# Optimization experiments

Hardware: AMD Instinct MI355X
Metric: run time of the kernel (lower is better)

Reference implementation:

```python
import jax, jax.numpy as jnp
import numpy as np

B, IN, H0, H1, OUT = 4096, 1024, 4096, 4096, 1024
QMAX = 127.0


def setup_inputs() -> dict:
    key = jax.random.key(0)
    k0, k1, k2, k3 = jax.random.split(key, 4)
    x = jax.random.normal(k0, (B, IN), dtype=jnp.float32)
    # Linear weights hold already-quantized integer values (module casts .int())
    W0 = jax.random.randint(k1, (H0, IN + 1), -127, 128).astype(jnp.int32)
    W1 = jax.random.randint(k2, (H1, H0 + 1), -127, 128).astype(jnp.int32)
    W2 = jax.random.randint(k3, (OUT, H1 + 1), -127, 128).astype(jnp.int32)
    return {
        "x": x,
        "a_in0": jnp.float32(4.0), "a_w0": jnp.float32(0.05),
        "a_in2": jnp.float32(50.0), "a_w2": jnp.float32(0.05),
        "a_in4": jnp.float32(50.0), "a_w4": jnp.float32(0.05),
        "W0": W0, "W1": W1, "W2": W2,
    }


def _quant(x, amax):
    # clamp(round(x * 127/amax), -127, 127) -> int32
    return jnp.clip(jnp.round(x * (QMAX / amax)), -QMAX, QMAX).astype(jnp.int32)


def _qlinear(x, W, a_in, a_w):
    q = _quant(x, a_in)                                   # [B, K] int32
    ones = jnp.ones((q.shape[0], 1), dtype=jnp.int32)     # folded bias column
    q = jnp.concatenate([q, ones], axis=1)                # [B, K+1]
    acc = q @ W.T                                         # int32 GEMM [B, N]
    return acc.astype(jnp.float32) * (a_w * a_in / (QMAX * QMAX))


def reference(x, a_in0, a_w0, a_in2, a_w2, a_in4, a_w4, W0, W1, W2):
    x = x.reshape(x.shape[0], -1)
    x = _qlinear(x, W0, a_in0, a_w0)
    x = jax.nn.relu(x)
    x = _qlinear(x, W1, a_in2, a_w2)
    x = jax.nn.relu(x)
    x = _qlinear(x, W2, a_in4, a_w4)
    return x
```

## Files before the change

### kernel.cpp

```cpp
#include <hip/hip_runtime.h>

#define QMAX 127.0f

typedef int v4i __attribute__((ext_vector_type(4)));

__device__ __forceinline__ void gload_lds16(const void* g, void* l) {
  __builtin_amdgcn_global_load_lds(
      (const __attribute__((address_space(1))) void*)g,
      (__attribute__((address_space(3))) void*)l, 16, 0, 0);
}

__device__ __forceinline__ void pack_body(const int* __restrict__ W,
                                          signed char* __restrict__ W8,
                                          int* __restrict__ bias,
                                          unsigned lblk, int kshift) {
  unsigned t = lblk * 256u + threadIdx.x;
  unsigned row = t >> kshift;
  unsigned j = t & ((1u << kshift) - 1u);
  unsigned K = 4u << kshift;
  size_t srcBase = (size_t)row * (size_t)(K + 1) + (size_t)j * 4;
  int c0 = W[srcBase + 0], c1 = W[srcBase + 1], c2 = W[srcBase + 2], c3 = W[srcBase + 3];
  unsigned packed = (unsigned)(c0 & 0xff) | ((unsigned)(c1 & 0xff) << 8) |
                    ((unsigned)(c2 & 0xff) << 16) | ((unsigned)(c3 & 0xff) << 24);
  reinterpret_cast<unsigned*>(W8)[t] = packed;
  if (j == 0) bias[row] = W[(size_t)row * (K + 1) + K];
}

__global__ void prep_kernel(const float* __restrict__ x,
                            signed char* __restrict__ qa0,
                            const float* __restrict__ pAin,
                            const int* __restrict__ W0, signed char* __restrict__ W0p, int* __restrict__ b0,
                            const int* __restrict__ W1, signed char* __restrict__ W1p, int* __restrict__ b1,
                            const int* __restrict__ W2, signed char* __restrict__ W2p, int* __restrict__ b2) {
  unsigned blk = blockIdx.x;
  if (blk < 4096u) {
    pack_body(W0, W0p, b0, blk, 8);
  } else if (blk < 20480u) {
    pack_body(W1, W1p, b1, blk - 4096u, 10);
  } else if (blk < 24576u) {
    pack_body(W2, W2p, b2, blk - 20480u, 10);
  } else {
    unsigned t = (blk - 24576u) * 256u + threadIdx.x;
    float s = QMAX / pAin[0];
    float4 v = reinterpret_cast<const float4*>(x)[t];
    int q0 = (int)fminf(fmaxf(rintf(v.x * s), -QMAX), QMAX);
    int q1 = (int)fminf(fmaxf(rintf(v.y * s), -QMAX), QMAX);
    int q2 = (int)fminf(fmaxf(rintf(v.z * s), -QMAX), QMAX);
    int q3 = (int)fminf(fmaxf(rintf(v.w * s), -QMAX), QMAX);
    unsigned packed = (unsigned)(q0 & 0xff) | ((unsigned)(q1 & 0xff) << 8) |
                      ((unsigned)(q2 & 0xff) << 16) | ((unsigned)(q3 & 0xff) << 24);
    reinterpret_cast<unsigned*>(qa0)[t] = packed;
  }
}


#define FENCE() asm volatile("" ::: "memory")
#define BARRIER()                      \
  do {                                 \
    FENCE();                           \
    __builtin_amdgcn_s_barrier();      \
    FENCE();                           \
  } while (0)
#define LGK(n) asm volatile("s_waitcnt lgkmcnt(" #n ")" ::: "memory")
#define VMC(n) asm volatile("s_waitcnt vmcnt(" #n ")" ::: "memory")

#define STG128(bf, t)                                                         \
  do {                                                                        \
    _Pragma("unroll") for (int ii = 0; ii < 4; ++ii) {                        \
      int c = ii * 256 + tid;                                                 \
      int r = c >> 3;                                                         \
      int osrc = ((c & 7) << 4) ^ ((r & 7) << 4);                             \
      gload_lds16(A + (size_t)(browBase + r) * K + ((t) * 128 + osrc),        \
                  ldsA + (bf) * 16384 + c * 16);                              \
      gload_lds16(Bw + (size_t)(bcolBase + r) * K + ((t) * 128 + osrc),       \
                  ldsB + (bf) * 16384 + c * 16);                              \
    }                                                                         \
  } while (0)

#define LDA4_128(bf, kk, dst)                                                 \
  do {                                                                        \
    _Pragma("unroll") for (int m = 0; m < 4; ++m) {                           \
      int row = wr + m * 16 + l15;                                            \
      int off = ((kk) * 64 + hi * 16) ^ ((l15 & 7) << 4);                     \
      dst[m] = *(const v4i*)(ldsA + (bf) * 16384 + row * 128 + off);          \
    }                                                                         \
  } while (0)

#define LDB4_128(bf, kk)                                                      \
  do {                                                                        \
    _Pragma("unroll") for (int n = 0; n < 4; ++n) {                           \
      int row = wc + n * 16 + l15;                                            \
      int off = ((kk) * 64 + hi * 16) ^ ((l15 & 7) << 4);                     \
      bK[n] = *(const v4i*)(ldsB + (bf) * 16384 + row * 128 + off);           \
    }                                                                         \
  } while (0)

#define MFMA16(aset)                                                          \
  do {                                                                        \
    __builtin_amdgcn_s_setprio(1);                                            \
    _Pragma("unroll") for (int m = 0; m < 4; ++m)                             \
    _Pragma("unroll") for (int n = 0; n < 4; ++n)                             \
      acc[m][n] = __builtin_amdgcn_mfma_i32_16x16x64_i8(                      \
          aset[m], bK[n], acc[m][n], 0, 0, 0);                                \
    __builtin_amdgcn_s_setprio(0);                                            \
  } while (0)

template <int MODE>
__global__ __launch_bounds__(256)
void qgemm_kernel(const signed char* __restrict__ A,
                  const signed char* __restrict__ Bw,
                  const int* __restrict__ bias,
                  void* __restrict__ outp,
                  int N, int K, int nbn,
                  const float* __restrict__ pAin,
                  const float* __restrict__ pAw,
                  const float* __restrict__ pAnext) {
  __shared__ signed char slds[65536];
  signed char* ldsA = slds;
  signed char* ldsB = slds + 32768;

  const int nwg = gridDim.x, bid = blockIdx.x, per = nwg >> 3;
  const int swz = (bid & 7) * per + (bid >> 3);
  const int brow = swz / nbn, bcol = swz - brow * nbn;
  const int browBase = brow << 7, bcolBase = bcol << 7;

  const int tid = threadIdx.x;
  const int lane = tid & 63, l15 = lane & 15, hi = lane >> 4;
  const int wid = tid >> 6;
  const int wr = (wid >> 1) << 6, wc = (wid & 1) << 6;

  v4i acc[4][4] = {};
  v4i aK0[4], aK1[4], bK[4];

  const int nk = K >> 7, niter = nk >> 1, nkm = nk - 1;

  STG128(0, 0);
  VMC(0);
  BARRIER();
  LDA4_128(0, 0, aK0);

#pragma unroll 1
  for (int i = 0; i < niter; ++i) {
    const int tO = 2 * i + 1;
    const int tE = (2 * i + 2) & nkm;
    LGK(4);
    BARRIER();
    STG128(1, tO);
    LDB4_128(0, 0); FENCE(); LDA4_128(0, 1, aK1);
    LGK(4);
    MFMA16(aK0);
    VMC(0);
    BARRIER();
    LDB4_128(0, 1); FENCE(); LDA4_128(1, 0, aK0);
    LGK(4);
    MFMA16(aK1);
    LGK(4);
    BARRIER();
    STG128(0, tE);
    LDB4_128(1, 0); FENCE(); LDA4_128(1, 1, aK1);
    LGK(4);
    MFMA16(aK0);
    VMC(0);
    BARRIER();
    LDB4_128(1, 1); FENCE(); LDA4_128(0, 0, aK0);
    LGK(4);
    MFMA16(aK1);
  }

  VMC(0);

  const float sDeq = (pAw[0] * pAin[0]) / (QMAX * QMAX);
  if (MODE == 0) {
    const float sQ = QMAX / pAnext[0];
    signed char* O = reinterpret_cast<signed char*>(outp);
#pragma unroll
    for (int n = 0; n < 4; ++n) {
      int gcol = bcolBase + wc + n * 16 + l15;
      int bv = bias[gcol];
#pragma unroll
      for (int m = 0; m < 4; ++m) {
        int growb = browBase + wr + m * 16 + (hi << 2);
#pragma unroll
        for (int r = 0; r < 4; ++r) {
          float f = (float)(acc[m][n][r] + bv) * sDeq;
          f = fmaxf(f, 0.0f);
          float qf = fminf(fmaxf(rintf(f * sQ), -QMAX), QMAX);
          O[(size_t)(growb + r) * N + gcol] = (signed char)(int)qf;
        }
      }
    }
  } else {
    float* O = reinterpret_cast<float*>(outp);
#pragma unroll
    for (int n = 0; n < 4; ++n) {
      int gcol = bcolBase + wc + n * 16 + l15;
      int bv = bias[gcol];
#pragma unroll
      for (int m = 0; m < 4; ++m) {
        int growb = browBase + wr + m * 16 + (hi << 2);
#pragma unroll
        for (int r = 0; r < 4; ++r) {
          O[(size_t)(growb + r) * N + gcol] = (float)(acc[m][n][r] + bv) * sDeq;
        }
      }
    }
  }
}

extern "C" void kernel_launch(void* const* d_in, const int* in_sizes, int n_in,
                              void* d_out, int out_size, void* d_ws, size_t ws_size,
                              hipStream_t stream) {
  const float* x     = (const float*)d_in[0];
  const float* a_in0 = (const float*)d_in[1];
  const float* a_w0  = (const float*)d_in[2];
  const float* a_in2 = (const float*)d_in[3];
  const float* a_w2  = (const float*)d_in[4];
  const float* a_in4 = (const float*)d_in[5];
  const float* a_w4  = (const float*)d_in[6];
  const int*   W0    = (const int*)d_in[7];
  const int*   W1    = (const int*)d_in[8];
  const int*   W2    = (const int*)d_in[9];
  float* out = (float*)d_out;

  constexpr int B = 4096, IN = 1024, H0 = 4096, H1 = 4096, OUTN = 1024;

  char* ws = (char*)d_ws;
  size_t off = 0;
  auto alloc = [&](size_t sz) {
    char* p = ws + off;
    off += (sz + 255) & ~(size_t)255;
    return p;
  };
  signed char* qa0 = (signed char*)alloc((size_t)B * IN);
  signed char* qa1 = (signed char*)alloc((size_t)B * H0);
  signed char* qa2 = (signed char*)alloc((size_t)B * H1);
  signed char* W0p = (signed char*)alloc((size_t)H0 * IN);
  signed char* W1p = (signed char*)alloc((size_t)H1 * H0);
  signed char* W2p = (signed char*)alloc((size_t)OUTN * H1);
  int* b0 = (int*)alloc((size_t)H0 * 4);
  int* b1 = (int*)alloc((size_t)H1 * 4);
  int* b2 = (int*)alloc((size_t)OUTN * 4);

  prep_kernel<<<28672, 256, 0, stream>>>(x, qa0, a_in0,
                                         W0, W0p, b0,
                                         W1, W1p, b1,
                                         W2, W2p, b2);

  qgemm_kernel<0><<<(B / 128) * (H0 / 128), 256, 0, stream>>>(
      qa0, W0p, b0, qa1, H0, IN, H0 / 128, a_in0, a_w0, a_in2);

  qgemm_kernel<0><<<(B / 128) * (H1 / 128), 256, 0, stream>>>(
      qa1, W1p, b1, qa2, H1, H0, H1 / 128, a_in2, a_w2, a_in4);

  qgemm_kernel<1><<<(B / 128) * (OUTN / 128), 256, 0, stream>>>(
      qa2, W2p, b2, out, OUTN, H1, OUTN / 128, a_in4, a_w4, a_in4);
}
```

Before: 148.1 us.

## Use 256x256 tiles with 128KB LDS for the two int8 ReLU-quant GEMMs

Adds a new int8 GEMM kernel with 256x256 output tiles per workgroup. Each wave owns a 128x128 sub-tile of 8x8 MFMA fragments, and the kernel uses 128KB of dynamic LDS with double-buffered A/B stages and register double-buffering of the fragments. The first two layers switch to this kernel to raise arithmetic intensity and cut global/LDS traffic per MFMA. The last fp32-output layer keeps the 128x128 kernel. The trade-offs are one workgroup per CU, far fewer workgroups (256 for 4096x4096), and heavy register pressure from 64 accumulators.

Result: no change. 148.5 us (+0.3%).

```diff
diff --git a/kernel.cpp b/kernel.cpp
--- a/kernel.cpp
+++ b/kernel.cpp
@@ -53,7 +53,6 @@
   }
 }
 
-
 #define FENCE() asm volatile("" ::: "memory")
 #define BARRIER()                      \
   do {                                 \
@@ -64,15 +63,137 @@
 #define LGK(n) asm volatile("s_waitcnt lgkmcnt(" #n ")" ::: "memory")
 #define VMC(n) asm volatile("s_waitcnt vmcnt(" #n ")" ::: "memory")
 
+
+#define STG4(gbase, ldsbuf, t)                                                \
+  do {                                                                        \
+    _Pragma("unroll") for (int s = 0; s < 8; ++s)                             \
+      gload_lds16(gbase + (size_t)(s * 32) * K + (size_t)(t) * 128,           \
+                  (ldsbuf) + s * 4096 + tid * 16);                            \
+  } while (0)
+
+#define LDA8k(bf, kk, dst)                                                    \
+  do {                                                                        \
+    _Pragma("unroll") for (int m = 0; m < 8; ++m) {                           \
+      int row = wm * 128 + m * 16 + l15;                                      \
+      int off = ((kk) * 64 + hi * 16) ^ ((row & 7) << 4);                     \
+      dst[m] = *(const v4i*)(ldsA + (bf) * 32768 + row * 128 + off);          \
+    }                                                                         \
+  } while (0)
+
+#define LDB8k(bf, kk, dst)                                                    \
+  do {                                                                        \
+    _Pragma("unroll") for (int n = 0; n < 8; ++n) {                           \
+      int row = wn * 128 + n * 16 + l15;                                      \
+      int off = ((kk) * 64 + hi * 16) ^ ((row & 7) << 4);                     \
+      dst[n] = *(const v4i*)(ldsB + (bf) * 32768 + row * 128 + off);          \
+    }                                                                         \
+  } while (0)
+
+#define MFMA64(aset, bset)                                                    \
+  do {                                                                        \
+    __builtin_amdgcn_s_setprio(1);                                            \
+    _Pragma("unroll") for (int m = 0; m < 8; ++m)                             \
+    _Pragma("unroll") for (int n = 0; n < 8; ++n)                             \
+      acc[m][n] = __builtin_amdgcn_mfma_i32_16x16x64_i8(                      \
+          aset[m], bset[n], acc[m][n], 0, 0, 0);                              \
+    __builtin_amdgcn_s_setprio(0);                                            \
+  } while (0)
+
+__global__ __launch_bounds__(256, 1)
+void qgemm4w_kernel(const signed char* __restrict__ A,
+                    const signed char* __restrict__ Bw,
+                    const int* __restrict__ bias,
+                    signed char* __restrict__ O,
+                    int N, int K, int nbn,
+                    const float* __restrict__ pAin,
+                    const float* __restrict__ pAw,
+                    const float* __restrict__ pAnext) {
+  extern __shared__ signed char lds[];
+  signed char* ldsA = lds;
+  signed char* ldsB = lds + 65536;
+
+  const int nwg = gridDim.x, bid = blockIdx.x, per = nwg >> 3;
+  const int swz = (bid & 7) * per + (bid >> 3);
+  const int brow = swz / nbn, bcol = swz - brow * nbn;
+  const int browBase = brow << 8, bcolBase = bcol << 8;
+
+  const int tid = threadIdx.x;
+  const int lane = tid & 63, l15 = lane & 15, hi = lane >> 4;
+  const int wid = tid >> 6, wm = wid >> 1, wn = wid & 1;
+
+  const int r0 = tid >> 3;
+  const int osrc = ((tid & 7) ^ (r0 & 7)) << 4;
+  const signed char* gA = A + (size_t)(browBase + r0) * K + osrc;
+  const signed char* gB = Bw + (size_t)(bcolBase + r0) * K + osrc;
+
+  v4i acc[8][8] = {};
+  v4i aR0[8], bR0[8], aR1[8], bR1[8];
+
+  const int nk = K >> 7, niter = nk >> 1, nkm = nk - 1;
+
+  STG4(gA, ldsA, 0); STG4(gB, ldsB, 0);
+  VMC(0);
+  BARRIER();
+  LDA8k(0, 0, aR0); LDB8k(0, 0, bR0);
+  STG4(gA, ldsA + 32768, 1); STG4(gB, ldsB + 32768, 1);
+
+#pragma unroll 1
+  for (int i = 0; i < niter; ++i) {
+    const int tE = (2 * i + 2) & nkm;
+    const int tN = (2 * i + 3) & nkm;
+    LDA8k(0, 1, aR1); LDB8k(0, 1, bR1);
+    LGK(15);
+    MFMA64(aR0, bR0);
+    VMC(0);
+    BARRIER();
+    LDA8k(1, 0, aR0); LDB8k(1, 0, bR0);
+    LGK(15);
+    MFMA64(aR1, bR1);
+    BARRIER();
+    STG4(gA, ldsA, tE); STG4(gB, ldsB, tE);
+    LDA8k(1, 1, aR1); LDB8k(1, 1, bR1);
+    LGK(15);
+    MFMA64(aR0, bR0);
+    VMC(0);
+    BARRIER();
+    LDA8k(0, 0, aR0); LDB8k(0, 0, bR0);
+    LGK(15);
+    MFMA64(aR1, bR1);
+    BARRIER();
+    STG4(gA, ldsA + 32768, tN); STG4(gB, ldsB + 32768, tN);
+  }
+
+  VMC(0); LGK(0);
+
+  const float sDeq = (pAw[0] * pAin[0]) / (QMAX * QMAX);
+  const float sQ = QMAX / pAnext[0];
+#pragma unroll
+  for (int nf = 0; nf < 8; ++nf) {
+    const int gcol = bcolBase + wn * 128 + nf * 16 + l15;
+    const int bv = bias[gcol];
+#pragma unroll
+    for (int mf = 0; mf < 8; ++mf) {
+      const int gr = browBase + wm * 128 + mf * 16 + (hi << 2);
+#pragma unroll
+      for (int r = 0; r < 4; ++r) {
+        float f = (float)(acc[mf][nf][r] + bv) * sDeq;
+        f = fmaxf(f, 0.0f);
+        float qf = fminf(fmaxf(rintf(f * sQ), -QMAX), QMAX);
+        O[(size_t)(gr + r) * N + gcol] = (signed char)(int)qf;
+      }
+    }
+  }
+}
+
 #define STG128(bf, t)                                                         \
   do {                                                                        \
     _Pragma("unroll") for (int ii = 0; ii < 4; ++ii) {                        \
       int c = ii * 256 + tid;                                                 \
       int r = c >> 3;                                                         \
-      int osrc = ((c & 7) << 4) ^ ((r & 7) << 4);                             \
-      gload_lds16(A + (size_t)(browBase + r) * K + ((t) * 128 + osrc),        \
+      int osrc2 = ((c & 7) << 4) ^ ((r & 7) << 4);                            \
+      gload_lds16(A + (size_t)(browBase + r) * K + ((t) * 128 + osrc2),       \
                   ldsA + (bf) * 16384 + c * 16);                              \
-      gload_lds16(Bw + (size_t)(bcolBase + r) * K + ((t) * 128 + osrc),       \
+      gload_lds16(Bw + (size_t)(bcolBase + r) * K + ((t) * 128 + osrc2),      \
                   ldsB + (bf) * 16384 + c * 16);                              \
     }                                                                         \
   } while (0)
@@ -81,7 +202,7 @@
   do {                                                                        \
     _Pragma("unroll") for (int m = 0; m < 4; ++m) {                           \
       int row = wr + m * 16 + l15;                                            \
-      int off = ((kk) * 64 + hi * 16) ^ ((l15 & 7) << 4);                     \
+      int off = ((kk) * 64 + hi * 16) ^ ((row & 7) << 4);                     \
       dst[m] = *(const v4i*)(ldsA + (bf) * 16384 + row * 128 + off);          \
     }                                                                         \
   } while (0)
@@ -90,7 +211,7 @@
   do {                                                                        \
     _Pragma("unroll") for (int n = 0; n < 4; ++n) {                           \
       int row = wc + n * 16 + l15;                                            \
-      int off = ((kk) * 64 + hi * 16) ^ ((l15 & 7) << 4);                     \
+      int off = ((kk) * 64 + hi * 16) ^ ((row & 7) << 4);                     \
       bK[n] = *(const v4i*)(ldsB + (bf) * 16384 + row * 128 + off);           \
     }                                                                         \
   } while (0)
@@ -105,16 +226,14 @@
     __builtin_amdgcn_s_setprio(0);                                            \
   } while (0)
 
-template <int MODE>
 __global__ __launch_bounds__(256)
 void qgemm_kernel(const signed char* __restrict__ A,
                   const signed char* __restrict__ Bw,
                   const int* __restrict__ bias,
-                  void* __restrict__ outp,
+                  float* __restrict__ O,
                   int N, int K, int nbn,
                   const float* __restrict__ pAin,
-                  const float* __restrict__ pAw,
-                  const float* __restrict__ pAnext) {
+                  const float* __restrict__ pAw) {
   __shared__ signed char slds[65536];
   signed char* ldsA = slds;
   signed char* ldsB = slds + 32768;
@@ -170,38 +289,16 @@
   VMC(0);
 
   const float sDeq = (pAw[0] * pAin[0]) / (QMAX * QMAX);
-  if (MODE == 0) {
-    const float sQ = QMAX / pAnext[0];
-    signed char* O = reinterpret_cast<signed char*>(outp);
-#pragma unroll
-    for (int n = 0; n < 4; ++n) {
-      int gcol = bcolBase + wc + n * 16 + l15;
-      int bv = bias[gcol];
-#pragma unroll
-      for (int m = 0; m < 4; ++m) {
-        int growb = browBase + wr + m * 16 + (hi << 2);
-#pragma unroll
-        for (int r = 0; r < 4; ++r) {
-          float f = (float)(acc[m][n][r] + bv) * sDeq;
-          f = fmaxf(f, 0.0f);
-          float qf = fminf(fmaxf(rintf(f * sQ), -QMAX), QMAX);
-          O[(size_t)(growb + r) * N + gcol] = (signed char)(int)qf;
-        }
-      }
-    }
-  } else {
-    float* O = reinterpret_cast<float*>(outp);
-#pragma unroll
-    for (int n = 0; n < 4; ++n) {
-      int gcol = bcolBase + wc + n * 16 + l15;
-      int bv = bias[gcol];
-#pragma unroll
-      for (int m = 0; m < 4; ++m) {
-        int growb = browBase + wr + m * 16 + (hi << 2);
-#pragma unroll
-        for (int r = 0; r < 4; ++r) {
-          O[(size_t)(growb + r) * N + gcol] = (float)(acc[m][n][r] + bv) * sDeq;
-        }
+#pragma unroll
+  for (int n = 0; n < 4; ++n) {
+    int gcol = bcolBase + wc + n * 16 + l15;
+    int bv = bias[gcol];
+#pragma unroll
+    for (int m = 0; m < 4; ++m) {
+      int growb = browBase + wr + m * 16 + (hi << 2);
+#pragma unroll
+      for (int r = 0; r < 4; ++r) {
+        O[(size_t)(growb + r) * N + gcol] = (float)(acc[m][n][r] + bv) * sDeq;
       }
     }
   }
@@ -241,17 +338,20 @@
   int* b1 = (int*)alloc((size_t)H1 * 4);
   int* b2 = (int*)alloc((size_t)OUTN * 4);
 
+  hipFuncSetAttribute((const void*)qgemm4w_kernel,
+                      hipFuncAttributeMaxDynamicSharedMemorySize, 131072);
+
   prep_kernel<<<28672, 256, 0, stream>>>(x, qa0, a_in0,
                                          W0, W0p, b0,
                                          W1, W1p, b1,
                                          W2, W2p, b2);
 
-  qgemm_kernel<0><<<(B / 128) * (H0 / 128), 256, 0, stream>>>(
-      qa0, W0p, b0, qa1, H0, IN, H0 / 128, a_in0, a_w0, a_in2);
-
-  qgemm_kernel<0><<<(B / 128) * (H1 / 128), 256, 0, stream>>>(
-      qa1, W1p, b1, qa2, H1, H0, H1 / 128, a_in2, a_w2, a_in4);
-
-  qgemm_kernel<1><<<(B / 128) * (OUTN / 128), 256, 0, stream>>>(
-      qa2, W2p, b2, out, OUTN, H1, OUTN / 128, a_in4, a_w4, a_in4);
-}
+  qgemm4w_kernel<<<(B / 256) * (H0 / 256), 256, 131072, stream>>>(
+      qa0, W0p, b0, qa1, H0, IN, H0 / 256, a_in0, a_w0, a_in2);
+
+  qgemm4w_kernel<<<(B / 256) * (H1 / 256), 256, 131072, stream>>>(
+      qa1, W1p, b1, qa2, H1, H0, H1 / 256, a_in2, a_w2, a_in4);
+
+  qgemm_kernel<<<(B / 128) * (OUTN / 128), 256, 0, stream>>>(
+      qa2, W2p, b2, out, OUTN, H1, OUTN / 128, a_in4, a_w4);
+}
```
